# Kernel optimization log

Measured on AMD Instinct MI355X. Metric: run time of the kernel, lower is better.

## Reference

```python
import jax, jax.numpy as jnp
import numpy as np

IGNORE_INDEX = 255
LOG_CLAMP = 100.0  # torch BCE clamps log at -100, so -log(x) <= 100


def _neg_log(x, cond):
    # BCE(x, 1) = -log(x), with the torch clamp log(x) >= -100.
    x_safe = jnp.where(cond, jnp.maximum(x, 1e-38), 1.0)
    return jnp.where(cond, jnp.minimum(-jnp.log(x_safe), LOG_CLAMP), 0.0)


def setup_inputs() -> dict:
    key = jax.random.key(0)
    k1, k2 = jax.random.split(key)
    B, C, H, W, D = 1, 20, 256, 256, 32
    pred = jax.random.normal(k1, (B, C, H, W, D), dtype=jnp.float32)
    target = jax.random.randint(k2, (B, H, W, D), 0, C, dtype=jnp.int64)
    return {"pred": pred, "target": target}


def reference(pred, target):
    C = pred.shape[1]
    p = jax.nn.softmax(pred, axis=1)                      # [B,C,H,W,D]
    mask = (target != IGNORE_INDEX)                        # [B,H,W,D]

    # Flatten voxels: [N, C] probs, [N] labels, [N] mask.
    p_flat = jnp.moveaxis(p, 1, -1).reshape(-1, C)
    t_flat = target.reshape(-1)
    m_flat = mask.reshape(-1).astype(p.dtype)
    t_safe = jnp.where(mask.reshape(-1), t_flat, 0).astype(jnp.int32)

    # Per-class reductions in one pass (replaces the per-class python loop):
    # nominator[c] = sum_{masked, t==c} p_c ; ct_count[c] = |{masked, t==c}|
    p_at_t = jnp.take_along_axis(p_flat, t_safe[:, None], axis=1)[:, 0] * m_flat
    nominator = jax.ops.segment_sum(p_at_t, t_safe, num_segments=C)
    ct_count = jax.ops.segment_sum(m_flat, t_safe, num_segments=C)
    sum_p = jnp.einsum('nc,n->c', p_flat, m_flat)          # sum of p_c over masked
    n_masked = jnp.sum(m_flat)

    neg_count = n_masked - ct_count                        # sum(1 - ct)
    spec_num = n_masked - sum_p - ct_count + nominator     # sum((1-p)(1-ct))

    valid = ct_count > 0
    prec = nominator / jnp.maximum(sum_p, 1e-38)
    rec = nominator / jnp.maximum(ct_count, 1.0)
    spec = spec_num / jnp.maximum(neg_count, 1.0)

    loss_c = (_neg_log(prec, valid & (sum_p > 0))
              + _neg_log(rec, valid)
              + _neg_log(spec, valid & (neg_count > 0)))
    count = jnp.sum(valid.astype(p.dtype))
    return jnp.sum(loss_c) / count
```

## Files before the change

### kernel.cpp

```cpp
#include <hip/hip_runtime.h>
#include <math.h>

#define NCLS 20
#define IGNORE_IDX 255
#define LOG2E 1.4426950408889634f
#define NTHR 256
#define NSLOT 32

typedef float v4f __attribute__((ext_vector_type(4)));
typedef int v4i __attribute__((ext_vector_type(4)));

__device__ __forceinline__ float wave_reduce(float v) {
#pragma unroll
  for (int off = 32; off > 0; off >>= 1) v += __shfl_xor(v, off, 64);
  return v;
}

__device__ __forceinline__ float neg_log_clamped(float x, bool cond) {
  if (!cond) return 0.0f;
  float xs = fmaxf(x, 1e-38f);
  return fminf(-logf(xs), 100.0f);
}

__global__ __launch_bounds__(NTHR) void pass1(const float* __restrict__ pred,
                                              const int* __restrict__ target,
                                              float* __restrict__ ws, int N) {
  __shared__ float s_acc[3 * NCLS][32];
  const int tid = threadIdx.x;
  const int sl = tid & 31;

  {
    float* p = &s_acc[0][0];
    for (int i = tid; i < 3 * NCLS * 32; i += NTHR) p[i] = 0.0f;
  }
  __syncthreads();

  const int nq = N >> 2;
  const int q = blockIdx.x * NTHR + tid;

  if (q < nq) {
    const int n = q << 2;
    const v4i t4 = *reinterpret_cast<const v4i*>(target + n);

    v4f Z = (v4f)(0.0f);
    v4f pt = (v4f)(0.0f);
#pragma unroll
    for (int c = 0; c < NCLS; ++c) {
      const v4f x = *reinterpret_cast<const v4f*>(pred + (size_t)c * N + n);
#pragma unroll
      for (int j = 0; j < 4; ++j) {
        const float e = __builtin_amdgcn_exp2f(fminf(x[j], 80.0f) * LOG2E);
        Z[j] += e;
        pt[j] = (c == t4[j]) ? e : pt[j];
      }
    }

    v4f w;
#pragma unroll
    for (int j = 0; j < 4; ++j) {
      const bool msk = (t4[j] != IGNORE_IDX);
      w[j] = msk ? __builtin_amdgcn_rcpf(Z[j]) : 0.0f;
    }
#pragma unroll
    for (int j = 0; j < 4; ++j) {
      if (t4[j] != IGNORE_IDX) {
        atomicAdd(&s_acc[NCLS + t4[j]][sl], pt[j] * w[j]);
        atomicAdd(&s_acc[2 * NCLS + t4[j]][sl], 1.0f);
      }
    }

#pragma unroll
    for (int c = 0; c < NCLS; ++c) {
      const v4f x = *reinterpret_cast<const v4f*>(pred + (size_t)c * N + n);
      float v = 0.0f;
#pragma unroll
      for (int j = 0; j < 4; ++j)
        v += __builtin_amdgcn_exp2f(fminf(x[j], 80.0f) * LOG2E) * w[j];
      atomicAdd(&s_acc[c][sl], v);
    }
  }
  __syncthreads();

  if (tid < 3 * NCLS) {
    const float* row = s_acc[tid];
    float v = 0.0f;
#pragma unroll
    for (int i = 0; i < 32; ++i) v += row[(i + tid) & 31];
    atomicAdd(&ws[(size_t)(blockIdx.x & (NSLOT - 1)) * 64 + tid], v);
  }
}

__global__ __launch_bounds__(64) void pass2(const float* __restrict__ ws,
                                            float* __restrict__ out) {
  __shared__ float s[64];
  const int lane = threadIdx.x;
  float a = 0.0f;
#pragma unroll
  for (int r = 0; r < NSLOT; ++r) a += ws[r * 64 + lane];

  const float n_masked =
      wave_reduce((lane >= 2 * NCLS && lane < 3 * NCLS) ? a : 0.0f);

  s[lane] = a;
  __syncthreads();

  float loss = 0.0f, validf = 0.0f;
  if (lane < NCLS) {
    const float sump = s[lane];
    const float nom = s[NCLS + lane];
    const float cnt = s[2 * NCLS + lane];
    const bool valid = cnt > 0.0f;
    const float prec = nom / fmaxf(sump, 1e-38f);
    const float rec = nom / fmaxf(cnt, 1.0f);
    const float negc = n_masked - cnt;
    const float specn = n_masked - sump - cnt + nom;
    const float spec = specn / fmaxf(negc, 1.0f);
    loss = neg_log_clamped(prec, valid && (sump > 0.0f)) +
           neg_log_clamped(rec, valid) +
           neg_log_clamped(spec, valid && (negc > 0.0f));
    validf = valid ? 1.0f : 0.0f;
  }
  loss = wave_reduce(loss);
  validf = wave_reduce(validf);
  if (lane == 0) out[0] = loss / validf;
}

extern "C" void kernel_launch(void* const* d_in, const int* in_sizes, int n_in,
                              void* d_out, int out_size, void* d_ws, size_t ws_size,
                              hipStream_t stream) {
  const float* pred = (const float*)d_in[0];
  const int* target = (const int*)d_in[1];
  const int N = in_sizes[1];
  const int nq = N >> 2;
  const int nblk = (nq + NTHR - 1) / NTHR;

  hipMemsetAsync(d_ws, 0, NSLOT * 64 * sizeof(float), stream);
  pass1<<<nblk, NTHR, 0, stream>>>(pred, target, (float*)d_ws, N);
  pass2<<<1, 64, 0, stream>>>((const float*)d_ws, (float*)d_out);
}
```

Measured before the change: 294.8 us.

## Split classes across half-waves, cache exps in registers, use persistent grid

Each voxel pair is now handled by two lanes, one per half-wave, and each lane covers half of the 20 classes. The softmax denominator is combined with a cross-lane shuffle. Exponentials are kept in registers, so pred is no longer re-read and exp is not recomputed in a second sweep. Launch becomes a fixed 2048-block grid-stride loop with an occupancy hint of 8 blocks per CU. The intent is to remove the duplicate global loads and exp work and to cut register pressure per thread. The cost is narrower 8-byte vector loads and loop overhead.

```diff
diff --git a/kernel.cpp b/kernel.cpp
--- a/kernel.cpp
+++ b/kernel.cpp
@@ -2,13 +2,15 @@
 #include <math.h>
 
 #define NCLS 20
+#define HALFC 10
 #define IGNORE_IDX 255
 #define LOG2E 1.4426950408889634f
 #define NTHR 256
+#define NBLK 2048
 #define NSLOT 32
 
-typedef float v4f __attribute__((ext_vector_type(4)));
-typedef int v4i __attribute__((ext_vector_type(4)));
+typedef float v2f __attribute__((ext_vector_type(2)));
+typedef int v2i __attribute__((ext_vector_type(2)));
 
 __device__ __forceinline__ float wave_reduce(float v) {
 #pragma unroll
@@ -22,12 +24,17 @@
   return fminf(-logf(xs), 100.0f);
 }
 
-__global__ __launch_bounds__(NTHR) void pass1(const float* __restrict__ pred,
-                                              const int* __restrict__ target,
-                                              float* __restrict__ ws, int N) {
+__global__ __launch_bounds__(NTHR, 8) void pass1(const float* __restrict__ pred,
+                                                 const int* __restrict__ target,
+                                                 float* __restrict__ ws, int N,
+                                                 int iters) {
   __shared__ float s_acc[3 * NCLS][32];
   const int tid = threadIdx.x;
+  const int lane = tid & 63;
   const int sl = tid & 31;
+  const int c0 = (lane >> 5) * HALFC;
+  const int wid = tid >> 6;
+  const int npair = N >> 1;
 
   {
     float* p = &s_acc[0][0];
@@ -35,48 +42,52 @@
   }
   __syncthreads();
 
-  const int nq = N >> 2;
-  const int q = blockIdx.x * NTHR + tid;
+  for (int k = 0; k < iters; ++k) {
+    const int pair = (k * NBLK + (int)blockIdx.x) * (NTHR >> 1) + wid * 32 + sl;
+    const bool inb = (pair < npair);
 
-  if (q < nq) {
-    const int n = q << 2;
-    const v4i t4 = *reinterpret_cast<const v4i*>(target + n);
+    v2f e[HALFC];
+#pragma unroll
+    for (int i = 0; i < HALFC; ++i) e[i] = (v2f)(0.0f);
+    v2i t2 = {IGNORE_IDX, IGNORE_IDX};
+    v2f Z = (v2f)(0.0f), pt = (v2f)(0.0f);
 
-    v4f Z = (v4f)(0.0f);
-    v4f pt = (v4f)(0.0f);
+    if (inb) {
+      const int n = pair << 1;
+      t2 = *reinterpret_cast<const v2i*>(target + n);
 #pragma unroll
-    for (int c = 0; c < NCLS; ++c) {
-      const v4f x = *reinterpret_cast<const v4f*>(pred + (size_t)c * N + n);
+      for (int i = 0; i < HALFC; ++i) {
+        const v2f x =
+            *reinterpret_cast<const v2f*>(pred + (size_t)(c0 + i) * N + n);
 #pragma unroll
-      for (int j = 0; j < 4; ++j) {
-        const float e = __builtin_amdgcn_exp2f(fminf(x[j], 80.0f) * LOG2E);
-        Z[j] += e;
-        pt[j] = (c == t4[j]) ? e : pt[j];
+        for (int j = 0; j < 2; ++j) {
+          e[i][j] = __builtin_amdgcn_exp2f(fminf(x[j], 80.0f) * LOG2E);
+          Z[j] += e[i][j];
+          pt[j] = (c0 + i == t2[j]) ? e[i][j] : pt[j];
+        }
       }
     }
 
-    v4f w;
+    float w[2];
 #pragma unroll
-    for (int j = 0; j < 4; ++j) {
-      const bool msk = (t4[j] != IGNORE_IDX);
-      w[j] = msk ? __builtin_amdgcn_rcpf(Z[j]) : 0.0f;
-    }
-#pragma unroll
-    for (int j = 0; j < 4; ++j) {
-      if (t4[j] != IGNORE_IDX) {
-        atomicAdd(&s_acc[NCLS + t4[j]][sl], pt[j] * w[j]);
-        atomicAdd(&s_acc[2 * NCLS + t4[j]][sl], 1.0f);
-      }
+    for (int j = 0; j < 2; ++j) {
+      const float Zf = Z[j] + __shfl_xor(Z[j], 32, 64);
+      const bool val = inb && (t2[j] != IGNORE_IDX);
+      w[j] = val ? __builtin_amdgcn_rcpf(Zf) : 0.0f;
     }
 
 #pragma unroll
-    for (int c = 0; c < NCLS; ++c) {
-      const v4f x = *reinterpret_cast<const v4f*>(pred + (size_t)c * N + n);
-      float v = 0.0f;
+    for (int i = 0; i < HALFC; ++i)
+      atomicAdd(&s_acc[c0 + i][sl], e[i][0] * w[0] + e[i][1] * w[1]);
+
 #pragma unroll
-      for (int j = 0; j < 4; ++j)
-        v += __builtin_amdgcn_exp2f(fminf(x[j], 80.0f) * LOG2E) * w[j];
-      atomicAdd(&s_acc[c][sl], v);
+    for (int j = 0; j < 2; ++j) {
+      const int to = t2[j] - c0;
+      const bool val = inb && (t2[j] != IGNORE_IDX);
+      if (val && to >= 0 && to < HALFC) {
+        atomicAdd(&s_acc[NCLS + t2[j]][sl], pt[j] * w[j]);
+        atomicAdd(&s_acc[2 * NCLS + t2[j]][sl], 1.0f);
+      }
     }
   }
   __syncthreads();
@@ -131,10 +142,11 @@
   const float* pred = (const float*)d_in[0];
   const int* target = (const int*)d_in[1];
   const int N = in_sizes[1];
-  const int nq = N >> 2;
-  const int nblk = (nq + NTHR - 1) / NTHR;
+  const int npair = N >> 1;
+  const int per_iter = NBLK * (NTHR >> 1);
+  const int iters = (npair + per_iter - 1) / per_iter;
 
   hipMemsetAsync(d_ws, 0, NSLOT * 64 * sizeof(float), stream);
-  pass1<<<nblk, NTHR, 0, stream>>>(pred, target, (float*)d_ws, N);
+  pass1<<<NBLK, NTHR, 0, stream>>>(pred, target, (float*)d_ws, N, iters);
   pass2<<<1, 64, 0, stream>>>((const float*)d_ws, (float*)d_out);
 }
```

Result: slower. 305.3 us (+3.6%).

## Restructure pass1 into persistent tiled blocks with per-wave class ownership

Applied to the files above, without the earlier changes.

Pass1 now runs a fixed grid of persistent 640-thread blocks that loop over 512-voxel tiles. Each of the ten waves owns two classes: it loads and exponentiates pred once into LDS and adds to a shared denominator with LDS atomics. It then accumulates sum_p, nominator and count in registers and finishes with a wave reduction. This removes the second global read and exp pass over pred and the per-voxel LDS atomics into class bins. In exchange it adds LDS atomics on the denominator, about 42KB of LDS per block and three barriers per tile.

```diff
diff --git a/kernel.cpp b/kernel.cpp
--- a/kernel.cpp
+++ b/kernel.cpp
@@ -4,7 +4,9 @@
 #define NCLS 20
 #define IGNORE_IDX 255
 #define LOG2E 1.4426950408889634f
-#define NTHR 256
+#define NTHR 640
+#define TILEV 512
+#define NBLK 768
 #define NSLOT 32
 
 typedef float v4f __attribute__((ext_vector_type(4)));
@@ -25,68 +27,89 @@
 __global__ __launch_bounds__(NTHR) void pass1(const float* __restrict__ pred,
                                               const int* __restrict__ target,
                                               float* __restrict__ ws, int N) {
-  __shared__ float s_acc[3 * NCLS][32];
+  __shared__ float es[NCLS][TILEV];
+  __shared__ float zz[TILEV];
+  __shared__ int ts[TILEV];
   const int tid = threadIdx.x;
-  const int sl = tid & 31;
+  const int wid = tid >> 6;
+  const int lane = tid & 63;
 
-  {
-    float* p = &s_acc[0][0];
-    for (int i = tid; i < 3 * NCLS * 32; i += NTHR) p[i] = 0.0f;
-  }
-  __syncthreads();
+  float sp[2] = {0.0f, 0.0f}, nom[2] = {0.0f, 0.0f}, cnt[2] = {0.0f, 0.0f};
 
-  const int nq = N >> 2;
-  const int q = blockIdx.x * NTHR + tid;
+  const long long step = (long long)NBLK * TILEV;
+  for (long long t0 = (long long)blockIdx.x * TILEV; t0 < N; t0 += step) {
+    if (tid < TILEV) zz[tid] = 0.0f;
+    if (tid < TILEV / 4) {
+      const long long g = t0 + tid * 4;
+      const long long ga = g > (long long)N - 4 ? (long long)N - 4 : g;
+      const v4i t4 = *reinterpret_cast<const v4i*>(target + ga);
+#pragma unroll
+      for (int j = 0; j < 4; ++j)
+        ts[j * 128 + tid] = (g + j < N) ? t4[j] : IGNORE_IDX;
+    }
+    __syncthreads();
 
-  if (q < nq) {
-    const int n = q << 2;
-    const v4i t4 = *reinterpret_cast<const v4i*>(target + n);
+#pragma unroll
+    for (int pi = 0; pi < 2; ++pi) {
+      const int c = wid + pi * 10;
+#pragma unroll
+      for (int i = 0; i < 2; ++i) {
+        const long long g = t0 + i * 256 + lane * 4;
+        const long long ga = g > (long long)N - 4 ? (long long)N - 4 : g;
+        const v4f x = *reinterpret_cast<const v4f*>(pred + (size_t)c * N + ga);
+#pragma unroll
+        for (int j = 0; j < 4; ++j) {
+          float e = __builtin_amdgcn_exp2f(fminf(x[j], 80.0f) * LOG2E);
+          if (g + j >= N) e = 0.0f;
+          const int s = j * 128 + i * 64 + lane;
+          es[c][s] = e;
+          atomicAdd(&zz[s], e);
+        }
+      }
+    }
+    __syncthreads();
 
-    v4f Z = (v4f)(0.0f);
-    v4f pt = (v4f)(0.0f);
+    float rz[2][4];
+    int tv[2][4];
 #pragma unroll
-    for (int c = 0; c < NCLS; ++c) {
-      const v4f x = *reinterpret_cast<const v4f*>(pred + (size_t)c * N + n);
+    for (int i = 0; i < 2; ++i)
 #pragma unroll
       for (int j = 0; j < 4; ++j) {
-        const float e = __builtin_amdgcn_exp2f(fminf(x[j], 80.0f) * LOG2E);
-        Z[j] += e;
-        pt[j] = (c == t4[j]) ? e : pt[j];
+        const int s = j * 128 + i * 64 + lane;
+        rz[i][j] = __builtin_amdgcn_rcpf(zz[s]);
+        tv[i][j] = ts[s];
       }
+#pragma unroll
+    for (int pi = 0; pi < 2; ++pi) {
+      const int c = wid + pi * 10;
+#pragma unroll
+      for (int i = 0; i < 2; ++i)
+#pragma unroll
+        for (int j = 0; j < 4; ++j) {
+          const int s = j * 128 + i * 64 + lane;
+          const float p = es[c][s] * rz[i][j];
+          sp[pi] += (tv[i][j] != IGNORE_IDX) ? p : 0.0f;
+          if (tv[i][j] == c) {
+            nom[pi] += p;
+            cnt[pi] += 1.0f;
+          }
+        }
     }
-
-    v4f w;
-#pragma unroll
-    for (int j = 0; j < 4; ++j) {
-      const bool msk = (t4[j] != IGNORE_IDX);
-      w[j] = msk ? __builtin_amdgcn_rcpf(Z[j]) : 0.0f;
-    }
-#pragma unroll
-    for (int j = 0; j < 4; ++j) {
-      if (t4[j] != IGNORE_IDX) {
-        atomicAdd(&s_acc[NCLS + t4[j]][sl], pt[j] * w[j]);
-        atomicAdd(&s_acc[2 * NCLS + t4[j]][sl], 1.0f);
-      }
-    }
+    __syncthreads();
+  }
 
 #pragma unroll
-    for (int c = 0; c < NCLS; ++c) {
-      const v4f x = *reinterpret_cast<const v4f*>(pred + (size_t)c * N + n);
-      float v = 0.0f;
-#pragma unroll
-      for (int j = 0; j < 4; ++j)
-        v += __builtin_amdgcn_exp2f(fminf(x[j], 80.0f) * LOG2E) * w[j];
-      atomicAdd(&s_acc[c][sl], v);
+  for (int pi = 0; pi < 2; ++pi) {
+    const int c = wid + pi * 10;
+    const float s = wave_reduce(sp[pi]);
+    const float nm = wave_reduce(nom[pi]);
+    const float ct = wave_reduce(cnt[pi]);
+    if (lane == 0) {
+      float* row = ws + (size_t)(blockIdx.x & (NSLOT - 1)) * 64;
+      atomicAdd(row + c, s);
+      atomicAdd(row + NCLS + c, nm);
+      atomicAdd(row + 2 * NCLS + c, ct);
     }
-  }
-  __syncthreads();
-
-  if (tid < 3 * NCLS) {
-    const float* row = s_acc[tid];
-    float v = 0.0f;
-#pragma unroll
-    for (int i = 0; i < 32; ++i) v += row[(i + tid) & 31];
-    atomicAdd(&ws[(size_t)(blockIdx.x & (NSLOT - 1)) * 64 + tid], v);
   }
 }
 
@@ -107,13 +130,13 @@
   float loss = 0.0f, validf = 0.0f;
   if (lane < NCLS) {
     const float sump = s[lane];
-    const float nom = s[NCLS + lane];
-    const float cnt = s[2 * NCLS + lane];
-    const bool valid = cnt > 0.0f;
-    const float prec = nom / fmaxf(sump, 1e-38f);
-    const float rec = nom / fmaxf(cnt, 1.0f);
-    const float negc = n_masked - cnt;
-    const float specn = n_masked - sump - cnt + nom;
+    const float nm = s[NCLS + lane];
+    const float ct = s[2 * NCLS + lane];
+    const bool valid = ct > 0.0f;
+    const float prec = nm / fmaxf(sump, 1e-38f);
+    const float rec = nm / fmaxf(ct, 1.0f);
+    const float negc = n_masked - ct;
+    const float specn = n_masked - sump - ct + nm;
     const float spec = specn / fmaxf(negc, 1.0f);
     loss = neg_log_clamped(prec, valid && (sump > 0.0f)) +
            neg_log_clamped(rec, valid) +
@@ -131,10 +154,8 @@
   const float* pred = (const float*)d_in[0];
   const int* target = (const int*)d_in[1];
   const int N = in_sizes[1];
-  const int nq = N >> 2;
-  const int nblk = (nq + NTHR - 1) / NTHR;
 
   hipMemsetAsync(d_ws, 0, NSLOT * 64 * sizeof(float), stream);
-  pass1<<<nblk, NTHR, 0, stream>>>(pred, target, (float*)d_ws, N);
+  pass1<<<NBLK, NTHR, 0, stream>>>(pred, target, (float*)d_ws, N);
   pass2<<<1, 64, 0, stream>>>((const float*)d_ws, (float*)d_out);
 }
```

Result: slower. 438.5 us (+48.7%).
